# Kernel optimization log

Measured on AMD Instinct MI355X. Metric: run time of the kernel, lower is better.

## Reference

```python
import jax, jax.numpy as jnp
import numpy as np

TEMPERATURE = 0.5
NEG_FILL = -9000000000000000.0


def setup_inputs() -> dict:
    key = jax.random.key(0)
    z = jax.random.normal(key, (16384, 128), dtype=jnp.float32)
    return {"z": z}


def reference(z) -> jnp.ndarray:
    n2 = z.shape[0]  # 2N
    # L2 normalize rows (eps matches torch F.normalize default 1e-12)
    norm = jnp.maximum(jnp.linalg.norm(z, axis=1, keepdims=True), 1e-12)
    zn = z / norm
    # (2N, 2N) cosine similarity scaled by temperature
    sim = jnp.matmul(zn, zn.T) / TEMPERATURE
    # mask self-similarity on the diagonal
    idx = jnp.arange(n2)
    sim = jnp.where(idx[:, None] == idx[None, :], NEG_FILL, sim)
    # positive pair of row i is i^1 (2i <-> 2i+1)
    pos_indices = idx ^ 1
    pos_sim = sim[idx, pos_indices]
    loss = -pos_sim + jax.scipy.special.logsumexp(sim, axis=1)
    return jnp.mean(loss)
```

## Files before the change

kernel.cpp:

```cpp
#include <hip/hip_runtime.h>
#include <hip/hip_bf16.h>

#define N2 16384
#define D  128
#define PANEL 32768
#define C1   2.88539008177792681472f
#define SQC1 1.69864360258810896f
#define LN2  0.69314718055994530942f

typedef __bf16 bf16x8 __attribute__((ext_vector_type(8)));
typedef float  f32x4  __attribute__((ext_vector_type(4)));

#if __has_builtin(__builtin_amdgcn_exp2f)
#define EXP2(x) __builtin_amdgcn_exp2f(x)
#else
#define EXP2(x) exp2f(x)
#endif

__device__ __forceinline__ unsigned short f2bf(float f) {
    union { float f; unsigned u; } v; v.f = f;
    unsigned r = v.u + 0x7fffu + ((v.u >> 16) & 1u);
    return (unsigned short)(r >> 16);
}

__device__ __forceinline__ void stage_panel(const char* __restrict__ g,
                                            char* lds, int tid) {
    const int wid = tid >> 6, lane = tid & 63;
    #pragma unroll
    for (int i = 0; i < 8; ++i) {
        int off = (wid << 13) + (i << 10) + (lane << 4);
        int src = off ^ (((off >> 8) & 7) << 4);
        __builtin_amdgcn_global_load_lds(
            (const __attribute__((address_space(1))) unsigned*)(g + src),
            (__attribute__((address_space(3))) unsigned*)(lds + (wid << 13) + (i << 10)),
            16, 0, 0);
    }
}

__global__ void k_norm(const float* __restrict__ z, unsigned short* __restrict__ zn) {
    int row  = blockIdx.x * 4 + (threadIdx.x >> 6);
    int lane = threadIdx.x & 63;
    const float2 v = ((const float2*)(z + (size_t)row * D))[lane];
    float ss = v.x * v.x + v.y * v.y;
    #pragma unroll
    for (int m = 1; m < 64; m <<= 1) ss += __shfl_xor(ss, m);
    float inv = SQC1 / fmaxf(sqrtf(ss), 1e-12f);
    ushort2 o; o.x = f2bf(v.x * inv); o.y = f2bf(v.y * inv);
    ((ushort2*)(zn + (size_t)row * D))[lane] = o;
}

__global__ __launch_bounds__(256, 2)
void k_sim(const unsigned short* __restrict__ zn, float* __restrict__ rowsum) {
    __shared__ unsigned short ls[2][PANEL / 2];
    char* ls0 = (char*)&ls[0][0];
    char* ls1 = (char*)&ls[1][0];

    const int tileI = blockIdx.y;
    const int sBase = blockIdx.x * 16;
    const int nt = (blockIdx.x == 3 && tileI < 64) ? 17 : 16;
    const int tid  = threadIdx.x;
    const int lane = tid & 63, wid = tid >> 6;
    const int wr = wid >> 1, wc = wid & 1;
    const int l16 = lane & 15, lg = lane >> 4;
    const char* znb = (const char*)zn;
    const f32x4 ZERO = {0.f, 0.f, 0.f, 0.f};

    stage_panel(znb + (size_t)tileI * PANEL, ls0, tid);
    stage_panel(znb + (size_t)((tileI + sBase) & 127) * PANEL, ls1, tid);
    asm volatile("s_waitcnt vmcnt(8)" ::: "memory");
    __builtin_amdgcn_s_barrier();

    bf16x8 af[4][4];
    #pragma unroll
    for (int kk = 0; kk < 4; ++kk)
        #pragma unroll
        for (int m = 0; m < 4; ++m) {
            int row = wr * 64 + m * 16 + l16;
            int d = row * 256 + kk * 64 + lg * 16;
            af[kk][m] = *(const bf16x8*)(ls0 + (d ^ ((row & 7) << 4)));
        }
    asm volatile("s_waitcnt lgkmcnt(0)" ::: "memory");
    __builtin_amdgcn_s_barrier();

    float rs[4][4];
    #pragma unroll
    for (int m = 0; m < 4; ++m)
        #pragma unroll
        for (int r = 0; r < 4; ++r) rs[m][r] = 0.f;

    for (int t = 0; t < nt; ++t) {
        const int s  = sBase + t;
        const int jt = (tileI + s) & 127;
        char* rbuf = (t & 1) ? ls0 : ls1;
        char* sbuf = (t & 1) ? ls1 : ls0;
        if (t < nt - 1) {
            stage_panel(znb + (size_t)((tileI + s + 1) & 127) * PANEL, sbuf, tid);
            asm volatile("s_waitcnt vmcnt(8)" ::: "memory");
        } else {
            asm volatile("s_waitcnt vmcnt(0)" ::: "memory");
        }
        __builtin_amdgcn_s_barrier();

        bf16x8 bfr[4][4];
        #pragma unroll
        for (int kk = 0; kk < 4; ++kk)
            #pragma unroll
            for (int n = 0; n < 4; ++n) {
                int row = wc * 64 + n * 16 + l16;
                int d = row * 256 + kk * 64 + lg * 16;
                bfr[kk][n] = *(const bf16x8*)(rbuf + (d ^ ((row & 7) << 4)));
            }
        asm volatile("s_waitcnt lgkmcnt(0)" ::: "memory");
        __builtin_amdgcn_s_barrier();

        f32x4 acc[4][4];
        #pragma unroll
        for (int m = 0; m < 4; ++m)
            #pragma unroll
            for (int n = 0; n < 4; ++n)
                acc[m][n] = __builtin_amdgcn_mfma_f32_16x16x32_bf16(af[0][m], bfr[0][n], ZERO, 0, 0, 0);
        #pragma unroll
        for (int kk = 1; kk < 4; ++kk)
            #pragma unroll
            for (int m = 0; m < 4; ++m)
                #pragma unroll
                for (int n = 0; n < 4; ++n)
                    acc[m][n] = __builtin_amdgcn_mfma_f32_16x16x32_bf16(af[kk][m], bfr[kk][n], acc[m][n], 0, 0, 0);

        if (s == 0) {
            #pragma unroll
            for (int m = 0; m < 4; ++m)
                #pragma unroll
                for (int r = 0; r < 4; ++r) {
                    int li = wr * 64 + m * 16 + lg * 4 + r;
                    float a = 0.f;
                    #pragma unroll
                    for (int n = 0; n < 4; ++n) {
                        int lj = wc * 64 + n * 16 + l16;
                        float e = EXP2(acc[m][n][r]);
                        a += (li == lj) ? 0.f : e;
                    }
                    rs[m][r] += a;
                }
        } else {
            float cs[4] = {0.f, 0.f, 0.f, 0.f};
            #pragma unroll
            for (int m = 0; m < 4; ++m)
                #pragma unroll
                for (int r = 0; r < 4; ++r) {
                    float a = 0.f;
                    #pragma unroll
                    for (int n = 0; n < 4; ++n) {
                        float e = EXP2(acc[m][n][r]);
                        a += e;
                        cs[n] += e;
                    }
                    rs[m][r] += a;
                }
            #pragma unroll
            for (int n = 0; n < 4; ++n) {
                float v = cs[n];
                v += __shfl_xor(v, 16);
                v += __shfl_xor(v, 32);
                if (lg == 0)
                    atomicAdd(&rowsum[jt * 128 + wc * 64 + n * 16 + l16], v);
            }
        }
    }

    #pragma unroll
    for (int m = 0; m < 4; ++m)
        #pragma unroll
        for (int r = 0; r < 4; ++r) {
            float v = rs[m][r];
            v += __shfl_xor(v, 1);
            v += __shfl_xor(v, 2);
            v += __shfl_xor(v, 4);
            v += __shfl_xor(v, 8);
            if (l16 == 0)
                atomicAdd(&rowsum[tileI * 128 + wr * 64 + m * 16 + lg * 4 + r], v);
        }
}

__global__ void k_loss_reduce(const unsigned short* __restrict__ zn,
                              const float* __restrict__ rowsum,
                              float* __restrict__ out) {
    const int tid = threadIdx.x + blockIdx.x * 256;
    float p = 0.f;
    const bf16x8* v8 = (const bf16x8*)zn;
    for (int v = tid; v < N2 * D / 8; v += 64 * 256) {
        bf16x8 a = v8[v];
        bf16x8 b = v8[v ^ 16];
        #pragma unroll
        for (int e = 0; e < 8; ++e) p += (float)a[e] * (float)b[e];
    }
    float part = logf(rowsum[tid]) - LN2 * p;

    __shared__ float sm[4];
    #pragma unroll
    for (int m = 1; m < 64; m <<= 1) part += __shfl_xor(part, m);
    if ((threadIdx.x & 63) == 0) sm[threadIdx.x >> 6] = part;
    __syncthreads();
    if (threadIdx.x == 0)
        atomicAdd(out, (sm[0] + sm[1] + sm[2] + sm[3]) * (1.0f / (float)N2));
}

extern "C" void kernel_launch(void* const* d_in, const int* in_sizes, int n_in,
                              void* d_out, int out_size, void* d_ws, size_t ws_size,
                              hipStream_t stream) {
    const float* z = (const float*)d_in[0];
    float* out = (float*)d_out;

    unsigned short* zn = (unsigned short*)d_ws;
    float* rowsum = (float*)((char*)d_ws + (size_t)N2 * D * 2);

    hipMemsetAsync(rowsum, 0, N2 * sizeof(float), stream);
    hipMemsetAsync(out, 0, sizeof(float), stream);
    k_norm<<<N2 / 4, 256, 0, stream>>>(z, zn);
    dim3 grid(4, 128);
    k_sim<<<grid, 256, 0, stream>>>(zn, rowsum);
    k_loss_reduce<<<64, 256, 0, stream>>>(zn, rowsum, out);
}
```

Baseline: 68.50 us.

## Fold memsets into norm kernel, buffer column sums in LDS, rework pipeline

Drops the two hipMemsetAsync calls by zeroing rowsum and out inside k_norm. In k_sim, per-tile column partial sums now go to an LDS buffer through LDS atomics and are flushed to global rowsum once at the end, cutting global atomic traffic. The double-buffer schedule changes to one barrier per iteration with a full vmcnt(0) wait, and s_setprio is raised around the MFMA block. The risks are less load/compute overlap because of the stricter waits, and the extra LDS for colbuf may reduce occupancy.

```diff
diff --git a/kernel.cpp b/kernel.cpp
--- a/kernel.cpp
+++ b/kernel.cpp
@@ -4,7 +4,6 @@
 #define N2 16384
 #define D  128
 #define PANEL 32768
-#define C1   2.88539008177792681472f
 #define SQC1 1.69864360258810896f
 #define LN2  0.69314718055994530942f
 
@@ -37,7 +36,10 @@
     }
 }
 
-__global__ void k_norm(const float* __restrict__ z, unsigned short* __restrict__ zn) {
+__global__ void k_norm(const float* __restrict__ z, unsigned short* __restrict__ zn,
+                       float* __restrict__ rowsum, float* __restrict__ out) {
+    if (blockIdx.x < 64) rowsum[blockIdx.x * 256 + threadIdx.x] = 0.f;
+    if (blockIdx.x == 64 && threadIdx.x == 0) out[0] = 0.f;
     int row  = blockIdx.x * 4 + (threadIdx.x >> 6);
     int lane = threadIdx.x & 63;
     const float2 v = ((const float2*)(z + (size_t)row * D))[lane];
@@ -51,13 +53,16 @@
 
 __global__ __launch_bounds__(256, 2)
 void k_sim(const unsigned short* __restrict__ zn, float* __restrict__ rowsum) {
-    __shared__ unsigned short ls[2][PANEL / 2];
-    char* ls0 = (char*)&ls[0][0];
-    char* ls1 = (char*)&ls[1][0];
+    __shared__ char ls[2 * PANEL];
+    __shared__ float colbuf[17 * 128];
+    char* ls0 = ls;
+    char* ls1 = ls + PANEL;
 
     const int tileI = blockIdx.y;
-    const int sBase = blockIdx.x * 16;
-    const int nt = (blockIdx.x == 3 && tileI < 64) ? 17 : 16;
+    const int c = blockIdx.x;
+    const int sLo = c * 16;
+    const int nt = (c == 3 && tileI < 64) ? 17 : 16;
+
     const int tid  = threadIdx.x;
     const int lane = tid & 63, wid = tid >> 6;
     const int wr = wid >> 1, wc = wid & 1;
@@ -65,9 +70,11 @@
     const char* znb = (const char*)zn;
     const f32x4 ZERO = {0.f, 0.f, 0.f, 0.f};
 
+    #pragma unroll
+    for (int u = tid; u < 17 * 128; u += 256) colbuf[u] = 0.f;
+
     stage_panel(znb + (size_t)tileI * PANEL, ls0, tid);
-    stage_panel(znb + (size_t)((tileI + sBase) & 127) * PANEL, ls1, tid);
-    asm volatile("s_waitcnt vmcnt(8)" ::: "memory");
+    asm volatile("s_waitcnt vmcnt(0)" ::: "memory");
     __builtin_amdgcn_s_barrier();
 
     bf16x8 af[4][4];
@@ -82,6 +89,8 @@
     asm volatile("s_waitcnt lgkmcnt(0)" ::: "memory");
     __builtin_amdgcn_s_barrier();
 
+    stage_panel(znb + (size_t)((tileI + sLo) & 127) * PANEL, ls0, tid);
+
     float rs[4][4];
     #pragma unroll
     for (int m = 0; m < 4; ++m)
@@ -89,17 +98,15 @@
         for (int r = 0; r < 4; ++r) rs[m][r] = 0.f;
 
     for (int t = 0; t < nt; ++t) {
-        const int s  = sBase + t;
-        const int jt = (tileI + s) & 127;
-        char* rbuf = (t & 1) ? ls0 : ls1;
-        char* sbuf = (t & 1) ? ls1 : ls0;
-        if (t < nt - 1) {
+        const int s = sLo + t;
+
+        asm volatile("s_waitcnt vmcnt(0)" ::: "memory");
+        __builtin_amdgcn_s_barrier();
+
+        char* rbuf = (t & 1) ? ls1 : ls0;
+        char* sbuf = (t & 1) ? ls0 : ls1;
+        if (t + 1 < nt)
             stage_panel(znb + (size_t)((tileI + s + 1) & 127) * PANEL, sbuf, tid);
-            asm volatile("s_waitcnt vmcnt(8)" ::: "memory");
-        } else {
-            asm volatile("s_waitcnt vmcnt(0)" ::: "memory");
-        }
-        __builtin_amdgcn_s_barrier();
 
         bf16x8 bfr[4][4];
         #pragma unroll
@@ -110,10 +117,9 @@
                 int d = row * 256 + kk * 64 + lg * 16;
                 bfr[kk][n] = *(const bf16x8*)(rbuf + (d ^ ((row & 7) << 4)));
             }
-        asm volatile("s_waitcnt lgkmcnt(0)" ::: "memory");
-        __builtin_amdgcn_s_barrier();
 
         f32x4 acc[4][4];
+        __builtin_amdgcn_s_setprio(1);
         #pragma unroll
         for (int m = 0; m < 4; ++m)
             #pragma unroll
@@ -126,6 +132,7 @@
                 #pragma unroll
                 for (int n = 0; n < 4; ++n)
                     acc[m][n] = __builtin_amdgcn_mfma_f32_16x16x32_bf16(af[kk][m], bfr[kk][n], acc[m][n], 0, 0, 0);
+        __builtin_amdgcn_s_setprio(0);
 
         if (s == 0) {
             #pragma unroll
@@ -163,7 +170,7 @@
                 v += __shfl_xor(v, 16);
                 v += __shfl_xor(v, 32);
                 if (lg == 0)
-                    atomicAdd(&rowsum[jt * 128 + wc * 64 + n * 16 + l16], v);
+                    atomicAdd(&colbuf[t * 128 + wc * 64 + n * 16 + l16], v);
             }
         }
     }
@@ -180,6 +187,16 @@
             if (l16 == 0)
                 atomicAdd(&rowsum[tileI * 128 + wr * 64 + m * 16 + lg * 4 + r], v);
         }
+
+    asm volatile("s_waitcnt lgkmcnt(0)" ::: "memory");
+    __builtin_amdgcn_s_barrier();
+    for (int u = tid; u < nt * 128; u += 256) {
+        int t = u >> 7, col = u & 127;
+        int jt = (tileI + sLo + t) & 127;
+        float v = colbuf[u];
+        if (v != 0.f)
+            atomicAdd(&rowsum[jt * 128 + col], v);
+    }
 }
 
 __global__ void k_loss_reduce(const unsigned short* __restrict__ zn,
@@ -214,9 +231,7 @@
     unsigned short* zn = (unsigned short*)d_ws;
     float* rowsum = (float*)((char*)d_ws + (size_t)N2 * D * 2);
 
-    hipMemsetAsync(rowsum, 0, N2 * sizeof(float), stream);
-    hipMemsetAsync(out, 0, sizeof(float), stream);
-    k_norm<<<N2 / 4, 256, 0, stream>>>(z, zn);
+    k_norm<<<N2 / 4, 256, 0, stream>>>(z, zn, rowsum, out);
     dim3 grid(4, 128);
     k_sim<<<grid, 256, 0, stream>>>(zn, rowsum);
     k_loss_reduce<<<64, 256, 0, stream>>>(zn, rowsum, out);
```

Result: no change. 69.20 us (+1.0%).
